# Optimization experiments

Measured on AMD Instinct MI355X. Metric: run time of the kernel, lower is better.

Reference implementation:

```python
import jax, jax.numpy as jnp
import numpy as np

D_MODEL = 1024
NUM_HEADS = 16
D_K = D_MODEL // NUM_HEADS
THETA = 10000.0


def setup_inputs() -> dict:
    key = jax.random.key(0)
    ks = jax.random.split(key, 5)
    B, S = 2, 2048
    sigma = np.sqrt(2.0 / (D_MODEL + D_MODEL))
    x = jax.random.normal(ks[0], (B, S, D_MODEL), dtype=jnp.float32)
    Wq = jax.random.normal(ks[1], (D_MODEL, D_MODEL), dtype=jnp.float32) * sigma
    Wk = jax.random.normal(ks[2], (D_MODEL, D_MODEL), dtype=jnp.float32) * sigma
    Wv = jax.random.normal(ks[3], (D_MODEL, D_MODEL), dtype=jnp.float32) * sigma
    Wo = jax.random.normal(ks[4], (D_MODEL, D_MODEL), dtype=jnp.float32) * sigma
    return {"x": x, "Wq": Wq, "Wk": Wk, "Wv": Wv, "Wo": Wo}


def _rope(x, cos, sin):
    # x: [B, H, S, D_K]; cos/sin: [S, D_K//2] broadcast to [1, 1, S, D_K//2]
    x1 = x[..., ::2]
    x2 = x[..., 1::2]
    even = x1 * cos - x2 * sin
    odd = x1 * sin + x2 * cos
    return jnp.stack((even, odd), axis=-1).reshape(x.shape)


def reference(x, Wq, Wk, Wv, Wo):
    B, S, _ = x.shape
    # projections: weight is (out, in), applied as einsum('oi,...i->...o')
    q = jnp.einsum('oi,bsi->bso', Wq, x).reshape(B, S, NUM_HEADS, D_K).transpose(0, 2, 1, 3)
    k = jnp.einsum('oi,bsi->bso', Wk, x).reshape(B, S, NUM_HEADS, D_K).transpose(0, 2, 1, 3)
    v = jnp.einsum('oi,bsi->bso', Wv, x).reshape(B, S, NUM_HEADS, D_K).transpose(0, 2, 1, 3)
    # RoPE tables (token_positions = arange(S))
    inv_freq = 1.0 / (THETA ** (jnp.arange(0, D_K, 2, dtype=jnp.float32) / D_K))
    t = jnp.arange(S, dtype=jnp.float32)
    freqs = t[:, None] * inv_freq[None, :]          # [S, D_K/2]
    cos = jnp.cos(freqs)[None, None]                # [1,1,S,D_K/2]
    sin = jnp.sin(freqs)[None, None]
    q = _rope(q, cos, sin)
    k = _rope(k, cos, sin)
    # causal attention, full materialized scores (faithful to source)
    scores = jnp.einsum('bhid,bhjd->bhij', q, k) / np.sqrt(D_K).astype(np.float32)
    causal = jnp.tril(jnp.ones((S, S), dtype=bool))
    scores = jnp.where(causal, scores, -jnp.inf)
    attn = jax.nn.softmax(scores, axis=-1)
    out = jnp.einsum('bhij,bhjd->bhid', attn, v)    # [B,H,S,D_K]
    out = out.transpose(0, 2, 1, 3).reshape(B, S, D_MODEL)
    return jnp.einsum('oi,bsi->bso', Wo, out)
```

## Files before the change

kernel.cpp:

```cpp
#include <hip/hip_runtime.h>

#define D_MODEL 1024
#define NUM_HEADS 16
#define SEQ 2048
#define BATCH 2

typedef __attribute__((ext_vector_type(8))) short bf16x8;
typedef __attribute__((ext_vector_type(4))) float f32x4;

__device__ __forceinline__ float bf2f(unsigned short u) {
    return __uint_as_float(((unsigned int)u) << 16);
}
__device__ __forceinline__ unsigned short f2bf(float f) {
    unsigned int u = __float_as_uint(f);
    return (unsigned short)((u + 0x7FFFu + ((u >> 16) & 1u)) >> 16);
}
__device__ __forceinline__ ushort4 pack4(float4 v) {
    return make_ushort4(f2bf(v.x), f2bf(v.y), f2bf(v.z), f2bf(v.w));
}

__device__ __forceinline__ void gload_lds16(const unsigned short* g, unsigned short* l) {
    __builtin_amdgcn_global_load_lds(
        (const __attribute__((address_space(1))) unsigned int*)g,
        (__attribute__((address_space(3))) unsigned int*)l,
        16, 0, 0);
}

__device__ __forceinline__ bf16x8 lds_read_swz(const unsigned short (*tile)[64], int row, int chunk) {
    const char* p = reinterpret_cast<const char*>(tile);
    return *reinterpret_cast<const bf16x8*>(p + row * 128 + (((chunk ^ (row & 7))) << 4));
}

__device__ __forceinline__ bf16x8 lds_read_swz32(const unsigned short (*tile)[32], int row, int chunk) {
    const char* p = reinterpret_cast<const char*>(tile);
    return *reinterpret_cast<const bf16x8*>(p + row * 64 + (((chunk ^ ((row >> 1) & 3))) << 4));
}

__device__ __forceinline__ bf16x8 lds_read_swz128(const unsigned short (*tile)[128], int row, int chunk) {
    const char* p = reinterpret_cast<const char*>(tile);
    return *reinterpret_cast<const bf16x8*>(p + row * 256 + (((chunk ^ (row & 15))) << 4));
}

__global__ __launch_bounds__(256) void conv_kernel(
    const float* __restrict__ src, unsigned short* __restrict__ dst, int n4)
{
    int i = blockIdx.x * 256 + threadIdx.x;
    if (i < n4) {
        float4 v = reinterpret_cast<const float4*>(src)[i];
        reinterpret_cast<ushort4*>(dst)[i] = pack4(v);
    }
}

__global__ __launch_bounds__(256) void conv4_kernel(
    const float* __restrict__ x, const float* __restrict__ Wq,
    const float* __restrict__ Wk, const float* __restrict__ Wv,
    unsigned short* __restrict__ xb, unsigned short* __restrict__ w3bf,
    float2* __restrict__ tab)
{
    int i = blockIdx.x * 256 + threadIdx.x;
    if (i < 1835008) {
        const float* src;
        unsigned short* dst;
        int off;
        if (i < 1048576) {
            src = x; dst = xb; off = i;
        } else {
            int j = i - 1048576;
            int which = j >> 18;
            off = j & 0x3FFFF;
            src = (which == 0) ? Wq : (which == 1) ? Wk : Wv;
            dst = w3bf + ((size_t)which << 20);
        }
        float4 v = reinterpret_cast<const float4*>(src)[off];
        reinterpret_cast<ushort4*>(dst)[off] = pack4(v);
    } else {
        int idx = i - 1835008;
        int s = idx >> 5, d2 = idx & 31;
        float inv = powf(10000.0f, -(float)d2 / 32.0f);
        float sn, cs;
        sincosf((float)s * inv, &sn, &cs);
        tab[idx] = make_float2(cs, sn);
    }
}

__global__ __launch_bounds__(256) void qkv_mfma_kernel(
    const unsigned short* __restrict__ xb,
    const unsigned short* __restrict__ w3,
    const float2* __restrict__ tab,
    unsigned short* __restrict__ qb, unsigned short* __restrict__ kb,
    unsigned short* __restrict__ vt)
{
    const int lin = blockIdx.x;
    const int b = lin & 7;
    const int t = lin >> 3;
    const int which = t % 3;
    const int y = t / 3;
    const unsigned short* __restrict__ W = w3 + (size_t)which * 1048576;
    const int m0 = y * 128;
    const int n0g = b * 128;

    __shared__ __align__(16) unsigned short As[2][128][32];
    __shared__ __align__(16) unsigned short Bs[2][128][32];

    const int tid = threadIdx.x;
    const int w = tid >> 6;
    const int lane = tid & 63;
    const int quad = lane >> 4;
    const int c15 = lane & 15;
    const int qm = w >> 1, qn = w & 1;
    const int srow4 = lane >> 2;
    const int sch4 = lane & 3;

    auto stage = [&](int k0, int buf) {
#pragma unroll
        for (int i = 0; i < 2; i++) {
            const int row = i * 64 + w * 16 + srow4;
            const int ch = sch4 ^ ((row >> 1) & 3);
            gload_lds16(xb + (size_t)(m0 + row) * 1024 + k0 + ch * 8,
                        &As[buf][i * 64 + w * 16][0]);
            gload_lds16(W + (size_t)(n0g + row) * 1024 + k0 + ch * 8,
                        &Bs[buf][i * 64 + w * 16][0]);
        }
    };

    f32x4 acc[4][4];
#pragma unroll
    for (int mi = 0; mi < 4; mi++)
#pragma unroll
        for (int ni = 0; ni < 4; ni++) acc[mi][ni] = (f32x4){0.f, 0.f, 0.f, 0.f};

    stage(0, 0);
    for (int k0 = 0; k0 < 1024; k0 += 32) {
        const int cb = (k0 >> 5) & 1;
        __syncthreads();
        if (k0 < 992) stage(k0 + 32, cb ^ 1);

        bf16x8 af[4], bfr[4];
#pragma unroll
        for (int mi = 0; mi < 4; mi++)
            af[mi] = lds_read_swz32(As[cb], qm * 64 + mi * 16 + c15, quad);
#pragma unroll
        for (int ni = 0; ni < 4; ni++)
            bfr[ni] = lds_read_swz32(Bs[cb], qn * 64 + ni * 16 + c15, quad);
#pragma unroll
        for (int mi = 0; mi < 4; mi++)
#pragma unroll
            for (int ni = 0; ni < 4; ni++)
                acc[mi][ni] = __builtin_amdgcn_mfma_f32_16x16x32_bf16(af[mi], bfr[ni], acc[mi][ni], 0, 0, 0);
    }

    __syncthreads();
    unsigned short* stg = &As[0][0][0] + w * (16 * 72);
    const int hq = b * 2 + qn;
    unsigned short* outp = (which == 0) ? qb : kb;
    const int odd = c15 & 1;

#pragma unroll
    for (int mi = 0; mi < 4; mi++) {
#pragma unroll
        for (int r = 0; r < 4; r++) {
            int m = m0 + qm * 64 + mi * 16 + quad * 4 + r;
            int s = m & (SEQ - 1);
            const float2* trow = tab + (s << 5);
#pragma unroll
            for (int ni = 0; ni < 4; ni++) {
                float val = acc[mi][ni][r];
                float res;
                if (which < 2) {
                    float part = __shfl_xor(val, 1);
                    float2 cs = trow[(ni * 16 + c15) >> 1];
                    res = odd ? (part * cs.y + val * cs.x) : (val * cs.x - part * cs.y);
                } else {
                    res = val;
                }
                stg[(quad * 4 + r) * 72 + ni * 16 + c15] = f2bf(res);
            }
        }
        if (which < 2) {
            int row = lane >> 2;
            int ch = lane & 3;
            int m = m0 + qm * 64 + mi * 16 + row;
            int s = m & (SEQ - 1);
            int bb = m >> 11;
            size_t ob = (((size_t)bb * NUM_HEADS + hq) * SEQ + s) * 64 + ch * 16;
            uint4 v0 = *reinterpret_cast<const uint4*>(&stg[row * 72 + ch * 16]);
            uint4 v1 = *reinterpret_cast<const uint4*>(&stg[row * 72 + ch * 16 + 8]);
            *reinterpret_cast<uint4*>(&outp[ob]) = v0;
            *reinterpret_cast<uint4*>(&outp[ob + 8]) = v1;
        } else {
            int mbase = m0 + qm * 64 + mi * 16;
            int bb = mbase >> 11;
            int s_base = mbase & (SEQ - 1);
            unsigned short tmp[16];
#pragma unroll
            for (int sl = 0; sl < 16; sl++) tmp[sl] = stg[sl * 72 + lane];
            size_t ob = (((size_t)bb * NUM_HEADS + hq) * 64 + lane) * SEQ + s_base;
            *reinterpret_cast<uint4*>(&vt[ob])     = *reinterpret_cast<uint4*>(&tmp[0]);
            *reinterpret_cast<uint4*>(&vt[ob + 8]) = *reinterpret_cast<uint4*>(&tmp[8]);
        }
    }
}

__global__ __launch_bounds__(512, 4) void attn_kernel(
    const unsigned short* __restrict__ qb, const unsigned short* __restrict__ kb,
    const unsigned short* __restrict__ vt, unsigned short* __restrict__ ab)
{
    const int xpair = blockIdx.x;
    const int bh = blockIdx.y;
    const int b = bh >> 4, h = bh & 15;
    const size_t base = (size_t)bh * SEQ * 64;
    const size_t vbase = (size_t)bh * 64 * SEQ;
    const int tid = threadIdx.x;
    const int w = tid >> 6;
    const int grp = w >> 2;
    const int wa = w & 3;
    const int lane = tid & 63;
    const int quad = lane >> 4;
    const int c15 = lane & 15;
    const int srow8 = lane >> 3;
    const int sch = lane & 7;
    const int srow16 = lane >> 4;
    const int sch16 = lane & 15;
    const float C = 0.125f;

    __shared__ __align__(16) unsigned short Ks[2][128][64];
    __shared__ __align__(16) unsigned short Vs[2][64][128];
    float* exch = (float*)&Ks[0][0][0];
    float2* ml  = (float2*)((char*)&Ks[0][0][0] + 17152);
    unsigned short* ost = &Vs[0][0][0];

    auto stage = [&](int sj, int buf) {
        const int j0s = sj * 128;
#pragma unroll
        for (int i = 0; i < 2; i++) {
            const int krow = w * 16 + i * 8 + srow8;
            const int kch = sch ^ (krow & 7);
            gload_lds16(kb + base + (size_t)(j0s + krow) * 64 + kch * 8,
                        &Ks[buf][w * 16 + i * 8][0]);
            const int vrow = w * 8 + i * 4 + srow16;
            const int vch = sch16 ^ (vrow & 15);
            gload_lds16(vt + vbase + (size_t)vrow * SEQ + j0s + vch * 8,
                        &Vs[buf][w * 8 + i * 4][0]);
        }
    };

    for (int pass = 0; pass < 2; pass++) {
        const int it = pass ? xpair : (31 - xpair);
        const int i0 = it * 64;
        const int nj = (it >> 1) + 1;

        const int qrow = i0 + wa * 16 + c15;
        bf16x8 qf0 = *reinterpret_cast<const bf16x8*>(&qb[base + (size_t)qrow * 64 + quad * 8]);
        bf16x8 qf1 = *reinterpret_cast<const bf16x8*>(&qb[base + (size_t)qrow * 64 + 32 + quad * 8]);

        float m_st = -1e30f, l_st = 0.f;
        f32x4 Oc[4];
#pragma unroll
        for (int t = 0; t < 4; t++) Oc[t] = (f32x4){0.f, 0.f, 0.f, 0.f};

        __syncthreads();
        stage(0, 0);

        for (int sj = 0; sj < nj; sj++) {
            const int cb = sj & 1;
            __syncthreads();
            if (sj < nj - 1) stage(sj + 1, cb ^ 1);

            const int j0 = sj * 128 + grp * 64;
            if (j0 <= i0) {
                bf16x8 kc0[4], kc1[4];
#pragma unroll
                for (int t = 0; t < 4; t++) {
                    kc0[t] = lds_read_swz(Ks[cb], grp * 64 + t * 16 + c15, quad);
                    kc1[t] = lds_read_swz(Ks[cb], grp * 64 + t * 16 + c15, 4 + quad);
                }

                f32x4 sc[4];
#pragma unroll
                for (int t = 0; t < 4; t++) sc[t] = (f32x4){0.f, 0.f, 0.f, 0.f};
                __builtin_amdgcn_s_setprio(1);
#pragma unroll
                for (int t = 0; t < 4; t++) {
                    sc[t] = __builtin_amdgcn_mfma_f32_16x16x32_bf16(kc0[t], qf0, sc[t], 0, 0, 0);
                    sc[t] = __builtin_amdgcn_mfma_f32_16x16x32_bf16(kc1[t], qf1, sc[t], 0, 0, 0);
                }
                __builtin_amdgcn_s_setprio(0);

                bf16x8 vv0[4], vv1[4];
#pragma unroll
                for (int t = 0; t < 4; t++) {
                    vv0[t] = lds_read_swz128(Vs[cb], t * 16 + c15, grp * 8 + quad);
                    vv1[t] = lds_read_swz128(Vs[cb], t * 16 + c15, grp * 8 + 4 + quad);
                }

                if (j0 == i0) {
                    const int gi = i0 + wa * 16 + c15;
#pragma unroll
                    for (int t = 0; t < 4; t++) {
#pragma unroll
                        for (int r = 0; r < 4; r++) {
                            int gj = j0 + t * 16 + quad * 4 + r;
                            if (gj > gi) sc[t][r] = -1e30f;
                        }
                    }
                }

                float x0 = fmaxf(fmaxf(sc[0][0], sc[0][1]), fmaxf(sc[0][2], sc[0][3]));
                float x1 = fmaxf(fmaxf(sc[1][0], sc[1][1]), fmaxf(sc[1][2], sc[1][3]));
                float x2 = fmaxf(fmaxf(sc[2][0], sc[2][1]), fmaxf(sc[2][2], sc[2][3]));
                float x3 = fmaxf(fmaxf(sc[3][0], sc[3][1]), fmaxf(sc[3][2], sc[3][3]));
                float tm = fmaxf(fmaxf(x0, x1), fmaxf(x2, x3));
                tm = fmaxf(tm, __shfl_xor(tm, 16));
                tm = fmaxf(tm, __shfl_xor(tm, 32));

                if (!__all(tm <= m_st + 64.0f)) {
                    float mnew = fmaxf(m_st, tm);
                    float alpha = __expf((m_st - mnew) * C);
                    l_st *= alpha;
#pragma unroll
                    for (int t = 0; t < 4; t++)
#pragma unroll
                        for (int r = 0; r < 4; r++) Oc[t][r] *= alpha;
                    m_st = mnew;
                }

                const float mC = m_st * C;
                float p[4][4];
#pragma unroll
                for (int t = 0; t < 4; t++)
#pragma unroll
                    for (int r = 0; r < 4; r++)
                        p[t][r] = __expf(__builtin_fmaf(sc[t][r], C, -mC));

                float s0 = (p[0][0] + p[0][1]) + (p[0][2] + p[0][3]);
                float s1 = (p[1][0] + p[1][1]) + (p[1][2] + p[1][3]);
                float s2 = (p[2][0] + p[2][1]) + (p[2][2] + p[2][3]);
                float s3 = (p[3][0] + p[3][1]) + (p[3][2] + p[3][3]);
                l_st += (s0 + s1) + (s2 + s3);

                unsigned int pk[4][2];
#pragma unroll
                for (int t = 0; t < 4; t++)
#pragma unroll
                    for (int hh = 0; hh < 2; hh++)
                        asm("v_cvt_pk_bf16_f32 %0, %1, %2"
                            : "=v"(pk[t][hh]) : "v"(p[t][2 * hh]), "v"(p[t][2 * hh + 1]));

                unsigned int w0[4], w1[4];
#pragma unroll
                for (int e = 0; e < 4; e++) {
                    int sl = c15 + 16 * ((2 * quad + (e >> 1)) & 3);
                    unsigned int a0 = (unsigned int)__shfl((int)pk[0][e & 1], sl);
                    unsigned int b0 = (unsigned int)__shfl((int)pk[1][e & 1], sl);
                    w0[e] = (quad >> 1) ? b0 : a0;
                    unsigned int a1 = (unsigned int)__shfl((int)pk[2][e & 1], sl);
                    unsigned int b1 = (unsigned int)__shfl((int)pk[3][e & 1], sl);
                    w1[e] = (quad >> 1) ? b1 : a1;
                }
                uint4 u0 = make_uint4(w0[0], w0[1], w0[2], w0[3]);
                uint4 u1 = make_uint4(w1[0], w1[1], w1[2], w1[3]);
                bf16x8 ap0 = *reinterpret_cast<bf16x8*>(&u0);
                bf16x8 ap1 = *reinterpret_cast<bf16x8*>(&u1);

                __builtin_amdgcn_s_setprio(1);
#pragma unroll
                for (int t = 0; t < 4; t++) {
                    Oc[t] = __builtin_amdgcn_mfma_f32_16x16x32_bf16(vv0[t], ap0, Oc[t], 0, 0, 0);
                    Oc[t] = __builtin_amdgcn_mfma_f32_16x16x32_bf16(vv1[t], ap1, Oc[t], 0, 0, 0);
                }
                __builtin_amdgcn_s_setprio(0);
            }
        }

        __syncthreads();
        float l_row = l_st;
        l_row += __shfl_xor(l_row, 16);
        l_row += __shfl_xor(l_row, 32);
        const int q = wa * 16 + c15;

        if (grp == 1) {
#pragma unroll
            for (int t = 0; t < 4; t++)
#pragma unroll
                for (int r = 0; r < 4; r++)
                    exch[q * 65 + t * 16 + quad * 4 + r] = Oc[t][r];
            if (quad == 0) ml[q] = make_float2(m_st, l_row);
        }
        __syncthreads();
        if (grp == 0) {
            float2 mlB = ml[q];
            float m = fmaxf(m_st, mlB.x);
            float aA = __expf((m_st - m) * C);
            float aB = __expf((mlB.x - m) * C);
            float inv = 1.0f / (l_row * aA + mlB.y * aB);
#pragma unroll
            for (int t = 0; t < 4; t++) {
#pragma unroll
                for (int hh = 0; hh < 2; hh++) {
                    float o0 = (Oc[t][2 * hh] * aA
                                + exch[q * 65 + t * 16 + quad * 4 + 2 * hh] * aB) * inv;
                    float o1 = (Oc[t][2 * hh + 1] * aA
                                + exch[q * 65 + t * 16 + quad * 4 + 2 * hh + 1] * aB) * inv;
                    unsigned int pko = (unsigned int)f2bf(o0) | ((unsigned int)f2bf(o1) << 16);
                    *reinterpret_cast<unsigned int*>(
                        &ost[q * 72 + t * 16 + quad * 4 + 2 * hh]) = pko;
                }
            }
            {
                int row = lane >> 2;
                int ch = lane & 3;
                int gi = i0 + wa * 16 + row;
                size_t ob = ((size_t)b * SEQ + gi) * 1024 + h * 64 + ch * 16;
                uint4 v0 = *reinterpret_cast<const uint4*>(&ost[(wa * 16 + row) * 72 + ch * 16]);
                uint4 v1 = *reinterpret_cast<const uint4*>(&ost[(wa * 16 + row) * 72 + ch * 16 + 8]);
                *reinterpret_cast<uint4*>(&ab[ob]) = v0;
                *reinterpret_cast<uint4*>(&ab[ob + 8]) = v1;
            }
        }
    }
}

__global__ __launch_bounds__(256) void out_mfma_kernel(
    const unsigned short* __restrict__ A, const unsigned short* __restrict__ Wob,
    float* __restrict__ out)
{
    const int lin = blockIdx.x;
    const int b = lin & 7;
    const int y = lin >> 3;
    const int m0 = y * 64;
    const int n0g = b * 128;

    __shared__ __align__(16) unsigned short As[2][64][32];
    __shared__ __align__(16) unsigned short Bs[2][128][32];

    const int tid = threadIdx.x;
    const int w = tid >> 6;
    const int lane = tid & 63;
    const int quad = lane >> 4;
    const int c15 = lane & 15;
    const int qm = w >> 1, qn = w & 1;
    const int srow4 = lane >> 2;
    const int sch4 = lane & 3;

    auto stage = [&](int k0, int buf) {
        {
            const int row = w * 16 + srow4;
            const int ch = sch4 ^ ((row >> 1) & 3);
            gload_lds16(A + (size_t)(m0 + row) * 1024 + k0 + ch * 8,
                        &As[buf][w * 16][0]);
        }
#pragma unroll
        for (int i = 0; i < 2; i++) {
            const int row = i * 64 + w * 16 + srow4;
            const int ch = sch4 ^ ((row >> 1) & 3);
            gload_lds16(Wob + (size_t)(n0g + row) * 1024 + k0 + ch * 8,
                        &Bs[buf][i * 64 + w * 16][0]);
        }
    };

    f32x4 acc[2][4];
#pragma unroll
    for (int mi = 0; mi < 2; mi++)
#pragma unroll
        for (int ni = 0; ni < 4; ni++) acc[mi][ni] = (f32x4){0.f, 0.f, 0.f, 0.f};

    stage(0, 0);
    for (int k0 = 0; k0 < 1024; k0 += 32) {
        const int cb = (k0 >> 5) & 1;
        __syncthreads();
        if (k0 < 992) stage(k0 + 32, cb ^ 1);

        bf16x8 af[2], bfr[4];
#pragma unroll
        for (int mi = 0; mi < 2; mi++)
            af[mi] = lds_read_swz32(As[cb], qm * 32 + mi * 16 + c15, quad);
#pragma unroll
        for (int ni = 0; ni < 4; ni++)
            bfr[ni] = lds_read_swz32(Bs[cb], qn * 64 + ni * 16 + c15, quad);
#pragma unroll
        for (int mi = 0; mi < 2; mi++)
#pragma unroll
            for (int ni = 0; ni < 4; ni++)
                acc[mi][ni] = __builtin_amdgcn_mfma_f32_16x16x32_bf16(af[mi], bfr[ni], acc[mi][ni], 0, 0, 0);
    }

#pragma unroll
    for (int mi = 0; mi < 2; mi++) {
#pragma unroll
        for (int r = 0; r < 4; r++) {
            int m = m0 + qm * 32 + mi * 16 + quad * 4 + r;
#pragma unroll
            for (int ni = 0; ni < 4; ni++) {
                int n = n0g + qn * 64 + ni * 16 + c15;
                out[(size_t)m * 1024 + n] = acc[mi][ni][r];
            }
        }
    }
}

extern "C" void kernel_launch(void* const* d_in, const int* in_sizes, int n_in,
                              void* d_out, int out_size, void* d_ws, size_t ws_size,
                              hipStream_t stream)
{
    const float* x  = (const float*)d_in[0];
    const float* Wq = (const float*)d_in[1];
    const float* Wk = (const float*)d_in[2];
    const float* Wv = (const float*)d_in[3];
    const float* Wo = (const float*)d_in[4];
    float* out = (float*)d_out;

    const size_t QKV_ELEMS = (size_t)BATCH * SEQ * D_MODEL;

    unsigned short* qb = (unsigned short*)d_ws;
    unsigned short* kb = qb + QKV_ELEMS;
    unsigned short* vt = kb + QKV_ELEMS;
    unsigned short* ab = vt + QKV_ELEMS;
    unsigned short* w3bf = ab;
    unsigned short* wobf = qb;
    unsigned short* xbuf = (unsigned short*)d_out;
    float2* tab = (float2*)((char*)d_out + 8 * 1024 * 1024);

    conv4_kernel<<<dim3(7424), 256, 0, stream>>>(x, Wq, Wk, Wv, xbuf, w3bf, tab);
    qkv_mfma_kernel<<<dim3(768), 256, 0, stream>>>(xbuf, w3bf, tab, qb, kb, vt);
    attn_kernel<<<dim3(16, 32), 512, 0, stream>>>(qb, kb, vt, ab);
    conv_kernel<<<dim3(1024), 256, 0, stream>>>(Wo, wobf, 262144);
    out_mfma_kernel<<<dim3(512), 256, 0, stream>>>(ab, wobf, out);
}
```

Measured before the change: 199.0 us.

## Software-pipeline QK^T of next tile with softmax and PV of previous tile

Result: slower. 225.4 us (+13.2%).

```diff
diff --git a/kernel.cpp b/kernel.cpp
--- a/kernel.cpp
+++ b/kernel.cpp
@@ -258,6 +258,89 @@
 #pragma unroll
         for (int t = 0; t < 4; t++) Oc[t] = (f32x4){0.f, 0.f, 0.f, 0.f};
 
+        f32x4 sc_p[4];
+        bf16x8 vv0_p[4], vv1_p[4];
+        int j0_p = -1;
+
+        auto softmax_pv = [&](int j0p) {
+            if (j0p == i0) {
+                const int gi = i0 + wa * 16 + c15;
+#pragma unroll
+                for (int t = 0; t < 4; t++) {
+#pragma unroll
+                    for (int r = 0; r < 4; r++) {
+                        int gj = j0p + t * 16 + quad * 4 + r;
+                        if (gj > gi) sc_p[t][r] = -1e30f;
+                    }
+                }
+            }
+
+            float x0 = fmaxf(fmaxf(sc_p[0][0], sc_p[0][1]), fmaxf(sc_p[0][2], sc_p[0][3]));
+            float x1 = fmaxf(fmaxf(sc_p[1][0], sc_p[1][1]), fmaxf(sc_p[1][2], sc_p[1][3]));
+            float x2 = fmaxf(fmaxf(sc_p[2][0], sc_p[2][1]), fmaxf(sc_p[2][2], sc_p[2][3]));
+            float x3 = fmaxf(fmaxf(sc_p[3][0], sc_p[3][1]), fmaxf(sc_p[3][2], sc_p[3][3]));
+            float tm = fmaxf(fmaxf(x0, x1), fmaxf(x2, x3));
+            tm = fmaxf(tm, __shfl_xor(tm, 16));
+            tm = fmaxf(tm, __shfl_xor(tm, 32));
+
+            if (!__all(tm <= m_st + 64.0f)) {
+                float mnew = fmaxf(m_st, tm);
+                float alpha = __expf((m_st - mnew) * C);
+                l_st *= alpha;
+#pragma unroll
+                for (int t = 0; t < 4; t++)
+#pragma unroll
+                    for (int r = 0; r < 4; r++) Oc[t][r] *= alpha;
+                m_st = mnew;
+            }
+
+            const float mC = m_st * C;
+            float p[4][4];
+#pragma unroll
+            for (int t = 0; t < 4; t++)
+#pragma unroll
+                for (int r = 0; r < 4; r++)
+                    p[t][r] = __expf(__builtin_fmaf(sc_p[t][r], C, -mC));
+
+            float s0 = (p[0][0] + p[0][1]) + (p[0][2] + p[0][3]);
+            float s1 = (p[1][0] + p[1][1]) + (p[1][2] + p[1][3]);
+            float s2 = (p[2][0] + p[2][1]) + (p[2][2] + p[2][3]);
+            float s3 = (p[3][0] + p[3][1]) + (p[3][2] + p[3][3]);
+            l_st += (s0 + s1) + (s2 + s3);
+
+            unsigned int pk[4][2];
+#pragma unroll
+            for (int t = 0; t < 4; t++)
+#pragma unroll
+                for (int hh = 0; hh < 2; hh++)
+                    asm("v_cvt_pk_bf16_f32 %0, %1, %2"
+                        : "=v"(pk[t][hh]) : "v"(p[t][2 * hh]), "v"(p[t][2 * hh + 1]));
+
+            unsigned int w0[4], w1[4];
+#pragma unroll
+            for (int e = 0; e < 4; e++) {
+                int sl = c15 + 16 * ((2 * quad + (e >> 1)) & 3);
+                unsigned int a0 = (unsigned int)__shfl((int)pk[0][e & 1], sl);
+                unsigned int b0 = (unsigned int)__shfl((int)pk[1][e & 1], sl);
+                w0[e] = (quad >> 1) ? b0 : a0;
+                unsigned int a1 = (unsigned int)__shfl((int)pk[2][e & 1], sl);
+                unsigned int b1 = (unsigned int)__shfl((int)pk[3][e & 1], sl);
+                w1[e] = (quad >> 1) ? b1 : a1;
+            }
+            uint4 u0 = make_uint4(w0[0], w0[1], w0[2], w0[3]);
+            uint4 u1 = make_uint4(w1[0], w1[1], w1[2], w1[3]);
+            bf16x8 ap0 = *reinterpret_cast<bf16x8*>(&u0);
+            bf16x8 ap1 = *reinterpret_cast<bf16x8*>(&u1);
+
+            __builtin_amdgcn_s_setprio(1);
+#pragma unroll
+            for (int t = 0; t < 4; t++) {
+                Oc[t] = __builtin_amdgcn_mfma_f32_16x16x32_bf16(vv0_p[t], ap0, Oc[t], 0, 0, 0);
+                Oc[t] = __builtin_amdgcn_mfma_f32_16x16x32_bf16(vv1_p[t], ap1, Oc[t], 0, 0, 0);
+            }
+            __builtin_amdgcn_s_setprio(0);
+        };
+
         __syncthreads();
         stage(0, 0);
 
@@ -267,110 +350,44 @@
             if (sj < nj - 1) stage(sj + 1, cb ^ 1);
 
             const int j0 = sj * 128 + grp * 64;
-            if (j0 <= i0) {
+            const bool cur = (j0 <= i0);
+
+            f32x4 sc_c[4];
+            if (cur) {
                 bf16x8 kc0[4], kc1[4];
 #pragma unroll
                 for (int t = 0; t < 4; t++) {
                     kc0[t] = lds_read_swz(Ks[cb], grp * 64 + t * 16 + c15, quad);
                     kc1[t] = lds_read_swz(Ks[cb], grp * 64 + t * 16 + c15, 4 + quad);
                 }
-
-                f32x4 sc[4];
-#pragma unroll
-                for (int t = 0; t < 4; t++) sc[t] = (f32x4){0.f, 0.f, 0.f, 0.f};
+#pragma unroll
+                for (int t = 0; t < 4; t++) sc_c[t] = (f32x4){0.f, 0.f, 0.f, 0.f};
                 __builtin_amdgcn_s_setprio(1);
 #pragma unroll
                 for (int t = 0; t < 4; t++) {
-                    sc[t] = __builtin_amdgcn_mfma_f32_16x16x32_bf16(kc0[t], qf0, sc[t], 0, 0, 0);
-                    sc[t] = __builtin_amdgcn_mfma_f32_16x16x32_bf16(kc1[t], qf1, sc[t], 0, 0, 0);
+                    sc_c[t] = __builtin_amdgcn_mfma_f32_16x16x32_bf16(kc0[t], qf0, sc_c[t], 0, 0, 0);
+                    sc_c[t] = __builtin_amdgcn_mfma_f32_16x16x32_bf16(kc1[t], qf1, sc_c[t], 0, 0, 0);
                 }
                 __builtin_amdgcn_s_setprio(0);
-
-                bf16x8 vv0[4], vv1[4];
+            }
+
+            if (j0_p >= 0) {
+                softmax_pv(j0_p);
+                j0_p = -1;
+            }
+
+            if (cur) {
+#pragma unroll
+                for (int t = 0; t < 4; t++) sc_p[t] = sc_c[t];
 #pragma unroll
                 for (int t = 0; t < 4; t++) {
-                    vv0[t] = lds_read_swz128(Vs[cb], t * 16 + c15, grp * 8 + quad);
-                    vv1[t] = lds_read_swz128(Vs[cb], t * 16 + c15, grp * 8 + 4 + quad);
+                    vv0_p[t] = lds_read_swz128(Vs[cb], t * 16 + c15, grp * 8 + quad);
+                    vv1_p[t] = lds_read_swz128(Vs[cb], t * 16 + c15, grp * 8 + 4 + quad);
                 }
-
-                if (j0 == i0) {
-                    const int gi = i0 + wa * 16 + c15;
-#pragma unroll
-                    for (int t = 0; t < 4; t++) {
-#pragma unroll
-                        for (int r = 0; r < 4; r++) {
-                            int gj = j0 + t * 16 + quad * 4 + r;
-                            if (gj > gi) sc[t][r] = -1e30f;
-                        }
-                    }
-                }
-
-                float x0 = fmaxf(fmaxf(sc[0][0], sc[0][1]), fmaxf(sc[0][2], sc[0][3]));
-                float x1 = fmaxf(fmaxf(sc[1][0], sc[1][1]), fmaxf(sc[1][2], sc[1][3]));
-                float x2 = fmaxf(fmaxf(sc[2][0], sc[2][1]), fmaxf(sc[2][2], sc[2][3]));
-                float x3 = fmaxf(fmaxf(sc[3][0], sc[3][1]), fmaxf(sc[3][2], sc[3][3]));
-                float tm = fmaxf(fmaxf(x0, x1), fmaxf(x2, x3));
-                tm = fmaxf(tm, __shfl_xor(tm, 16));
-                tm = fmaxf(tm, __shfl_xor(tm, 32));
-
-                if (!__all(tm <= m_st + 64.0f)) {
-                    float mnew = fmaxf(m_st, tm);
-                    float alpha = __expf((m_st - mnew) * C);
-                    l_st *= alpha;
-#pragma unroll
-                    for (int t = 0; t < 4; t++)
-#pragma unroll
-                        for (int r = 0; r < 4; r++) Oc[t][r] *= alpha;
-                    m_st = mnew;
-                }
-
-                const float mC = m_st * C;
-                float p[4][4];
-#pragma unroll
-                for (int t = 0; t < 4; t++)
-#pragma unroll
-                    for (int r = 0; r < 4; r++)
-                        p[t][r] = __expf(__builtin_fmaf(sc[t][r], C, -mC));
-
-                float s0 = (p[0][0] + p[0][1]) + (p[0][2] + p[0][3]);
-                float s1 = (p[1][0] + p[1][1]) + (p[1][2] + p[1][3]);
-                float s2 = (p[2][0] + p[2][1]) + (p[2][2] + p[2][3]);
-                float s3 = (p[3][0] + p[3][1]) + (p[3][2] + p[3][3]);
-                l_st += (s0 + s1) + (s2 + s3);
-
-                unsigned int pk[4][2];
-#pragma unroll
-                for (int t = 0; t < 4; t++)
-#pragma unroll
-                    for (int hh = 0; hh < 2; hh++)
-                        asm("v_cvt_pk_bf16_f32 %0, %1, %2"
-                            : "=v"(pk[t][hh]) : "v"(p[t][2 * hh]), "v"(p[t][2 * hh + 1]));
-
-                unsigned int w0[4], w1[4];
-#pragma unroll
-                for (int e = 0; e < 4; e++) {
-                    int sl = c15 + 16 * ((2 * quad + (e >> 1)) & 3);
-                    unsigned int a0 = (unsigned int)__shfl((int)pk[0][e & 1], sl);
-                    unsigned int b0 = (unsigned int)__shfl((int)pk[1][e & 1], sl);
-                    w0[e] = (quad >> 1) ? b0 : a0;
-                    unsigned int a1 = (unsigned int)__shfl((int)pk[2][e & 1], sl);
-                    unsigned int b1 = (unsigned int)__shfl((int)pk[3][e & 1], sl);
-                    w1[e] = (quad >> 1) ? b1 : a1;
-                }
-                uint4 u0 = make_uint4(w0[0], w0[1], w0[2], w0[3]);
-                uint4 u1 = make_uint4(w1[0], w1[1], w1[2], w1[3]);
-                bf16x8 ap0 = *reinterpret_cast<bf16x8*>(&u0);
-                bf16x8 ap1 = *reinterpret_cast<bf16x8*>(&u1);
-
-                __builtin_amdgcn_s_setprio(1);
-#pragma unroll
-                for (int t = 0; t < 4; t++) {
-                    Oc[t] = __builtin_amdgcn_mfma_f32_16x16x32_bf16(vv0[t], ap0, Oc[t], 0, 0, 0);
-                    Oc[t] = __builtin_amdgcn_mfma_f32_16x16x32_bf16(vv1[t], ap1, Oc[t], 0, 0, 0);
-                }
-                __builtin_amdgcn_s_setprio(0);
-            }
-        }
+                j0_p = j0;
+            }
+        }
+        if (j0_p >= 0) softmax_pv(j0_p);
 
         __syncthreads();
         float l_row = l_st;
```
